# Performance work log

Hardware: AMD Instinct MI355X
Metric: run time of the kernel (lower is better)

Reference implementation:

```python
import jax, jax.numpy as jnp
import numpy as np

HASH_BUCKETS = 1000
EMB_DIM = 16
LSTM_UNITS = 32
DENSE_UNITS = 32


def setup_inputs() -> dict:
    key = jax.random.key(0)
    ks = jax.random.split(key, 8)
    B, T = 4096, 512
    ids = jax.random.randint(ks[0], (B, T), 0, HASH_BUCKETS, dtype=jnp.int32)
    emb = jax.random.normal(ks[1], (HASH_BUCKETS, EMB_DIM), jnp.float32) * 0.05
    kernel = jax.random.normal(ks[2], (EMB_DIM, 4 * LSTM_UNITS), jnp.float32) * 0.1
    rec_kernel = jax.random.normal(ks[3], (LSTM_UNITS, 4 * LSTM_UNITS), jnp.float32) * 0.1
    w1 = jax.random.normal(ks[4], (LSTM_UNITS, DENSE_UNITS), jnp.float32) * 0.1
    b1 = jnp.zeros((DENSE_UNITS,), jnp.float32)
    w2 = jax.random.normal(ks[5], (DENSE_UNITS, 1), jnp.float32) * 0.1
    b2 = jnp.zeros((1,), jnp.float32)
    return {"ids": ids, "emb": emb, "kernel": kernel, "rec_kernel": rec_kernel,
            "w1": w1, "b1": b1, "w2": w2, "b2": b2}


def _lstm(x, kernel, rec_kernel):
    # x: [B, T, E]; Keras LSTM, use_bias=False, return last hidden state [B, H]
    B = x.shape[0]
    H = rec_kernel.shape[0]
    # precompute input projections for all timesteps: [T, B, 4H]
    xz = jnp.einsum('bte,ef->tbf', x, kernel)

    def step(carry, xz_t):
        h, c = carry
        z = xz_t + h @ rec_kernel  # [B, 4H]
        zi, zf, zc, zo = jnp.split(z, 4, axis=-1)  # Keras gate order i,f,c,o
        i = jax.nn.sigmoid(zi)
        f = jax.nn.sigmoid(zf)
        c = f * c + i * jnp.tanh(zc)
        o = jax.nn.sigmoid(zo)
        h = o * jnp.tanh(c)
        return (h, c), None

    init = (jnp.zeros((B, H), x.dtype), jnp.zeros((B, H), x.dtype))
    (h, _), _ = jax.lax.scan(step, init, xz)
    return h


def reference(ids, emb, kernel, rec_kernel, w1, b1, w2, b2):
    x = emb[ids]                        # [B, T, E] embedding lookup
    h = _lstm(x, kernel, rec_kernel)    # [B, H]
    y = jax.nn.relu(h @ w1 + b1)        # [B, 32]
    return y @ w2 + b2                  # [B, 1]
```

## Files before the change

kernel.cpp:

```cpp
#include <hip/hip_runtime.h>
#include <stdint.h>

#define HASH_BUCKETS 1000
#define EMB_DIM 16
#define HDIM 32
#define G4 128
#define TSTEPS 512
#define BATCH 4096

typedef short v8s __attribute__((ext_vector_type(8)));
typedef float v4f __attribute__((ext_vector_type(4)));
typedef float v2f __attribute__((ext_vector_type(2)));

__device__ __forceinline__ float frcp(float x) {
    float r; asm("v_rcp_f32 %0, %1" : "=v"(r) : "v"(x)); return r;
}
__device__ __forceinline__ float fexp2(float x) {
    float r; asm("v_exp_f32 %0, %1" : "=v"(r) : "v"(x)); return r;
}
__device__ __forceinline__ uint32_t cvtpk_bf16(float a, float b) {
    uint32_t r; asm("v_cvt_pk_bf16_f32 %0, %1, %2" : "=v"(r) : "v"(a), "v"(b)); return r;
}
__device__ __forceinline__ uint32_t bf16rne(float x) {
    uint32_t u = __float_as_uint(x);
    return (u + 0x7FFFu + ((u >> 16) & 1u)) >> 16;
}

__global__ void precompute_P2_kernel(const float* __restrict__ emb,
                                     const float* __restrict__ kern,
                                     float* __restrict__ P2) {
    int idx = blockIdx.x * blockDim.x + threadIdx.x;
    if (idx >= HASH_BUCKETS * G4) return;
    int row = idx >> 7;
    int c2  = idx & 127;
    int h = c2 >> 2;
    int g = c2 & 3;
    float acc = 0.f;
#pragma unroll
    for (int e = 0; e < EMB_DIM; ++e)
        acc = fmaf(emb[row * EMB_DIM + e], kern[e * G4 + g * 32 + h], acc);
    float sg = (g == 2) ? 2.8853900817779268f : -1.4426950408889634f;
    P2[idx] = acc * sg;
}

__global__ __launch_bounds__(256)
__attribute__((amdgpu_waves_per_eu(1, 1)))
void lstm_head_kernel(const int* __restrict__ ids,
                      const float* __restrict__ P2,
                      const float* __restrict__ R,
                      const float* __restrict__ w1,
                      const float* __restrict__ b1,
                      const float* __restrict__ w2,
                      const float* __restrict__ b2,
                      float* __restrict__ out) {
    __shared__ __align__(16) uint32_t hbuf[2][16][36];
    __shared__ float hfin[16][33];

    const int tid  = threadIdx.x;
    const int w    = tid >> 6;
    const int lane = tid & 63;
    const int col  = lane & 15;
    const int quad = lane >> 4;
    const int bb   = blockIdx.x * 16;
    const int u0   = 8 * w + 2 * quad;
    const int u1   = u0 + 1;

    const float PL2E   =  2.8853900817779268f;
    const float NL2E   = -1.4426950408889634f;
    const float N2PL2E = -5.7707801635558536f;

    union V8 { uint32_t u[4]; v8s v; };
    V8 A0, A1;
    {
        int tt = col >> 2, g = col & 3;
        float sg = (g == 2) ? PL2E : NL2E;
        int gc0 = g * 32 + 8 * w + 2 * tt;
        int gc1 = gc0 + 1;
#pragma unroll
        for (int r = 0; r < 4; ++r) {
            uint32_t h0p[2], h1p[2];
#pragma unroll
            for (int e = 0; e < 2; ++e) {
                int k = quad * 8 + 2 * r + e;
                h0p[e] = bf16rne(R[k * G4 + gc0] * sg);
                h1p[e] = bf16rne(R[k * G4 + gc1] * sg);
            }
            A0.u[r] = h0p[0] | (h0p[1] << 16);
            A1.u[r] = h1p[0] | (h1p[1] << 16);
        }
    }

    for (int i = tid; i < 2 * 16 * 36; i += 256)
        ((uint32_t*)hbuf)[i] = 0u;

    const uint32_t* rd[2] = { &hbuf[0][col][4 * quad],
                              &hbuf[1][col][4 * quad] };
    uint32_t* wr[2] = { &hbuf[1][col][4 * w + quad],
                        &hbuf[0][col][4 * w + quad] };

    const int* __restrict__ idrow = ids + (size_t)(bb + col) * TSTEPS;
    const float* __restrict__ baseL = P2 + 4 * u0;
    v4f xzE0, xzE1, xzO0, xzO1;
    {
        const float* p0 = baseL + (size_t)idrow[0] * G4;
        const float* p1 = baseL + (size_t)idrow[1] * G4;
        xzE0 = *(const v4f*)(p0);
        xzE1 = *(const v4f*)(p0 + 4);
        xzO0 = *(const v4f*)(p1);
        xzO1 = *(const v4f*)(p1 + 4);
    }
    int idE = idrow[2];
    int idO = idrow[3];

    v2f cc = {0.f, 0.f};
    v2f hv2 = {0.f, 0.f};

    __syncthreads();

    union V8R { uint4 q; v8s v; };

#define STEP(PB, XZ0, XZ1, IDX, T)                                              \
    {                                                                           \
                       \
        V8R Bhi;                                                                \
        Bhi.q = *(const uint4*)(rd[PB]);                                        \
              \
        v4f z0 = __builtin_amdgcn_mfma_f32_16x16x32_bf16(A0.v, Bhi.v, XZ0, 0, 0, 0); \
        v4f z1 = __builtin_amdgcn_mfma_f32_16x16x32_bf16(A1.v, Bhi.v, XZ1, 0, 0, 0); \
            \
        {                                                                       \
            const float* pf_ = baseL + (size_t)(IDX) * G4;                      \
            XZ0 = *(const v4f*)(pf_);                                           \
            XZ1 = *(const v4f*)(pf_ + 4);                                       \
        }                                                                       \
        { int nt_ = (T) + 4; IDX = idrow[nt_ < TSTEPS ? nt_ : (TSTEPS - 1)]; }  \
           \
        float ei0 = fexp2(z0[0]), ei1 = fexp2(z1[0]);                           \
        float ef0 = fexp2(z0[1]), ef1 = fexp2(z1[1]);                           \
        float eg0 = fexp2(z0[2]), eg1 = fexp2(z1[2]);                           \
        float eq0 = fexp2(z0[3]), eq1 = fexp2(z1[3]);                           \
        v2f di = v2f{ei0, ei1} + 1.f;                                           \
        v2f df = v2f{ef0, ef1} + 1.f;                                           \
        v2f dc = v2f{eg0, eg1} + 1.f;                                           \
        v2f dq = v2f{eq0, eq1} + 1.f;                                           \
        v2f Pp = di * df, Qq = dc * dq;                                         \
        v2f PQ = Pp * Qq;                                                       \
        float R4 = frcp(PQ.x * PQ.y);                                           \
        v2f rr; rr.x = R4 * PQ.y; rr.y = R4 * PQ.x;                             \
        v2f rP = rr * Qq, rQ = rr * Pp;                                         \
        v2f ig = rP * df, fg = rP * di, rc = rQ * dq, og = rQ * dc;             \
        v2f tz; tz.x = fmaf(N2PL2E, rc.x, PL2E);                                \
                tz.y = fmaf(N2PL2E, rc.y, PL2E);                                \
        v2f itz = ig * tz;                                                      \
        cc.x = fmaf(fg.x, cc.x, itz.x);                                         \
        cc.y = fmaf(fg.y, cc.y, itz.y);                                         \
        float ecc0 = fexp2(cc.x), ecc1 = fexp2(cc.y);                           \
        v2f dn = v2f{ecc0, ecc1} + 1.f;                                         \
        float R2 = frcp(dn.x * dn.y);                                           \
        v2f rn; rn.x = R2 * dn.y; rn.y = R2 * dn.x;                             \
        v2f m2og = og * (-2.f);                 \
        hv2.x = fmaf(m2og.x, rn.x, og.x);                                       \
        hv2.y = fmaf(m2og.y, rn.y, og.y);                                       \
               \
        wr[PB][0] = cvtpk_bf16(hv2.x, hv2.y);                                   \
                     \
        asm volatile("s_waitcnt lgkmcnt(0)\n\ts_barrier" ::: "memory");         \
    }

    for (int t = 0; t < TSTEPS; t += 2) {
        STEP(0, xzE0, xzE1, idE, t)
        STEP(1, xzO0, xzO1, idO, t + 1)
    }
#undef STEP

    hfin[col][u0] = hv2.x;
    hfin[col][u1] = hv2.y;
    __syncthreads();

    int u = tid & 31;
    for (int bq = tid >> 5; bq < 16; bq += 8) {
        float y = b1[u];
#pragma unroll
        for (int k = 0; k < HDIM; ++k)
            y = fmaf(hfin[bq][k], w1[k * HDIM + u], y);
        y = fmaxf(y, 0.f);
        float vv = y * w2[u];
#pragma unroll
        for (int off = 16; off >= 1; off >>= 1)
            vv += __shfl_xor(vv, off);
        if (u == 0) out[bb + bq] = vv + b2[0];
    }
}

extern "C" void kernel_launch(void* const* d_in, const int* in_sizes, int n_in,
                              void* d_out, int out_size, void* d_ws, size_t ws_size,
                              hipStream_t stream) {
    const int*   ids  = (const int*)d_in[0];
    const float* emb  = (const float*)d_in[1];
    const float* kern = (const float*)d_in[2];
    const float* rec  = (const float*)d_in[3];
    const float* w1   = (const float*)d_in[4];
    const float* b1   = (const float*)d_in[5];
    const float* w2   = (const float*)d_in[6];
    const float* b2   = (const float*)d_in[7];
    float* out = (float*)d_out;
    float* P2  = (float*)d_ws;

    precompute_P2_kernel<<<(HASH_BUCKETS * G4 + 255) / 256, 256, 0, stream>>>(
        emb, kern, P2);
    lstm_head_kernel<<<BATCH / 16, 256, 0, stream>>>(
        ids, P2, rec, w1, b1, w2, b2, out);
}
```

Before: 242.5 us.

## Replace LDS hidden-state exchange and block barrier with in-wave bpermute

Each wave now owns four batch rows and keeps the full recurrence inside the wave. The new hidden state is gathered with ds_bpermute instead of being written to LDS, which removes the block-wide s_barrier on every timestep. To cover all gate columns, each wave issues eight MFMAs per step with eight A fragments, then selects the relevant result by lane group. That is redundant matrix work and extra VGPR pressure traded for dropping the cross-wave synchronization.

```diff
diff --git a/kernel.cpp b/kernel.cpp
--- a/kernel.cpp
+++ b/kernel.cpp
@@ -53,16 +53,18 @@
                       const float* __restrict__ w2,
                       const float* __restrict__ b2,
                       float* __restrict__ out) {
-    __shared__ __align__(16) uint32_t hbuf[2][16][36];
     __shared__ float hfin[16][33];
 
     const int tid  = threadIdx.x;
     const int w    = tid >> 6;
     const int lane = tid & 63;
     const int col  = lane & 15;
-    const int quad = lane >> 4;
+    const int b    = col & 3;
+    const int d    = col >> 2;
+    const int q    = lane >> 4;
     const int bb   = blockIdx.x * 16;
-    const int u0   = 8 * w + 2 * quad;
+    const int batch = bb + 4 * w + b;
+    const int u0   = 8 * q + 2 * d;
     const int u1   = u0 + 1;
 
     const float PL2E   =  2.8853900817779268f;
@@ -70,35 +72,27 @@
     const float N2PL2E = -5.7707801635558536f;
 
     union V8 { uint32_t u[4]; v8s v; };
-    V8 A0, A1;
+    V8 A0, A1, A2, A3, A4, A5, A6, A7;
     {
-        int tt = col >> 2, g = col & 3;
-        float sg = (g == 2) ? PL2E : NL2E;
-        int gc0 = g * 32 + 8 * w + 2 * tt;
-        int gc1 = gc0 + 1;
-#pragma unroll
-        for (int r = 0; r < 4; ++r) {
-            uint32_t h0p[2], h1p[2];
-#pragma unroll
-            for (int e = 0; e < 2; ++e) {
-                int k = quad * 8 + 2 * r + e;
-                h0p[e] = bf16rne(R[k * G4 + gc0] * sg);
-                h1p[e] = bf16rne(R[k * G4 + gc1] * sg);
+        const float sg = (b == 2) ? PL2E : NL2E;
+        const int gbase = b * 32 + 8 * d;
+        V8* Aj[8] = { &A0, &A1, &A2, &A3, &A4, &A5, &A6, &A7 };
+#pragma unroll
+        for (int j = 0; j < 8; ++j) {
+#pragma unroll
+            for (int m = 0; m < 4; ++m) {
+                uint32_t p0 = bf16rne(R[(8 * q + 2 * m)     * G4 + gbase + j] * sg);
+                uint32_t p1 = bf16rne(R[(8 * q + 2 * m + 1) * G4 + gbase + j] * sg);
+                Aj[j]->u[m] = p0 | (p1 << 16);
             }
-            A0.u[r] = h0p[0] | (h0p[1] << 16);
-            A1.u[r] = h1p[0] | (h1p[1] << 16);
         }
     }
 
-    for (int i = tid; i < 2 * 16 * 36; i += 256)
-        ((uint32_t*)hbuf)[i] = 0u;
-
-    const uint32_t* rd[2] = { &hbuf[0][col][4 * quad],
-                              &hbuf[1][col][4 * quad] };
-    uint32_t* wr[2] = { &hbuf[1][col][4 * w + quad],
-                        &hbuf[0][col][4 * w + quad] };
-
-    const int* __restrict__ idrow = ids + (size_t)(bb + col) * TSTEPS;
+    const int adr = ((lane & 0x33)) << 2;
+
+    const bool deq0 = (d == 0), deq1 = (d == 1), deq2 = (d == 2);
+
+    const int* __restrict__ idrow = ids + (size_t)batch * TSTEPS;
     const float* __restrict__ baseL = P2 + 4 * u0;
     v4f xzE0, xzE1, xzO0, xzO1;
     {
@@ -114,27 +108,40 @@
 
     v2f cc = {0.f, 0.f};
     v2f hv2 = {0.f, 0.f};
-
-    __syncthreads();
+    uint32_t pk = 0u;
 
     union V8R { uint4 q; v8s v; };
 
-#define STEP(PB, XZ0, XZ1, IDX, T)                                              \
+#define STEP(XZ0, XZ1, IDX, T)                                                  \
     {                                                                           \
-                       \
-        V8R Bhi;                                                                \
-        Bhi.q = *(const uint4*)(rd[PB]);                                        \
-              \
-        v4f z0 = __builtin_amdgcn_mfma_f32_16x16x32_bf16(A0.v, Bhi.v, XZ0, 0, 0, 0); \
-        v4f z1 = __builtin_amdgcn_mfma_f32_16x16x32_bf16(A1.v, Bhi.v, XZ1, 0, 0, 0); \
             \
+        int B0_ = __builtin_amdgcn_ds_bpermute(adr,      (int)pk);              \
+        int B1_ = __builtin_amdgcn_ds_bpermute(adr + 16, (int)pk);              \
+        int B2_ = __builtin_amdgcn_ds_bpermute(adr + 32, (int)pk);              \
+        int B3_ = __builtin_amdgcn_ds_bpermute(adr + 48, (int)pk);              \
+        V8R Bv;                                                                 \
+        Bv.q.x = (uint32_t)B0_; Bv.q.y = (uint32_t)B1_;                         \
+        Bv.q.z = (uint32_t)B2_; Bv.q.w = (uint32_t)B3_;                         \
+                              \
+        v4f o0 = __builtin_amdgcn_mfma_f32_16x16x32_bf16(A0.v, Bv.v, XZ0, 0, 0, 0); \
+        v4f o1 = __builtin_amdgcn_mfma_f32_16x16x32_bf16(A1.v, Bv.v, XZ1, 0, 0, 0); \
+        v4f o2 = __builtin_amdgcn_mfma_f32_16x16x32_bf16(A2.v, Bv.v, XZ0, 0, 0, 0); \
+        v4f o3 = __builtin_amdgcn_mfma_f32_16x16x32_bf16(A3.v, Bv.v, XZ1, 0, 0, 0); \
+        v4f o4 = __builtin_amdgcn_mfma_f32_16x16x32_bf16(A4.v, Bv.v, XZ0, 0, 0, 0); \
+        v4f o5 = __builtin_amdgcn_mfma_f32_16x16x32_bf16(A5.v, Bv.v, XZ1, 0, 0, 0); \
+        v4f o6 = __builtin_amdgcn_mfma_f32_16x16x32_bf16(A6.v, Bv.v, XZ0, 0, 0, 0); \
+        v4f o7 = __builtin_amdgcn_mfma_f32_16x16x32_bf16(A7.v, Bv.v, XZ1, 0, 0, 0); \
+                 \
         {                                                                       \
             const float* pf_ = baseL + (size_t)(IDX) * G4;                      \
             XZ0 = *(const v4f*)(pf_);                                           \
             XZ1 = *(const v4f*)(pf_ + 4);                                       \
         }                                                                       \
         { int nt_ = (T) + 4; IDX = idrow[nt_ < TSTEPS ? nt_ : (TSTEPS - 1)]; }  \
-           \
+                \
+        v4f z0 = deq0 ? o0 : (deq1 ? o2 : (deq2 ? o4 : o6));                    \
+        v4f z1 = deq0 ? o1 : (deq1 ? o3 : (deq2 ? o5 : o7));                    \
+            \
         float ei0 = fexp2(z0[0]), ei1 = fexp2(z1[0]);                           \
         float ef0 = fexp2(z0[1]), ef1 = fexp2(z1[1]);                           \
         float eg0 = fexp2(z0[2]), eg1 = fexp2(z1[2]);                           \
@@ -158,23 +165,21 @@
         v2f dn = v2f{ecc0, ecc1} + 1.f;                                         \
         float R2 = frcp(dn.x * dn.y);                                           \
         v2f rn; rn.x = R2 * dn.y; rn.y = R2 * dn.x;                             \
-        v2f m2og = og * (-2.f);                 \
+        v2f m2og = og * (-2.f);                                                 \
         hv2.x = fmaf(m2og.x, rn.x, og.x);                                       \
         hv2.y = fmaf(m2og.y, rn.y, og.y);                                       \
-               \
-        wr[PB][0] = cvtpk_bf16(hv2.x, hv2.y);                                   \
-                     \
-        asm volatile("s_waitcnt lgkmcnt(0)\n\ts_barrier" ::: "memory");         \
+          \
+        pk = cvtpk_bf16(hv2.x, hv2.y);                                          \
     }
 
     for (int t = 0; t < TSTEPS; t += 2) {
-        STEP(0, xzE0, xzE1, idE, t)
-        STEP(1, xzO0, xzO1, idO, t + 1)
+        STEP(xzE0, xzE1, idE, t)
+        STEP(xzO0, xzO1, idO, t + 1)
     }
 #undef STEP
 
-    hfin[col][u0] = hv2.x;
-    hfin[col][u1] = hv2.y;
+    hfin[4 * w + b][u0] = hv2.x;
+    hfin[4 * w + b][u1] = hv2.y;
     __syncthreads();
 
     int u = tid & 31;
```

After: 288.3 us. +18.9%, slower.
